# Kernel optimization log

Measured on AMD Instinct MI355X. Metric: run time of the kernel, lower is better.

## Reference

```python
import jax, jax.numpy as jnp
import numpy as np

B, C4, N, L4 = 8, 64, 512, 12
CQ = C4 // 4  # conv output channels


def setup_inputs() -> dict:
    key = jax.random.key(0)
    k_x, k_wc, k_bc, k_wg, k_bg = jax.random.split(key, 5)
    x = jax.random.normal(k_x, (B, C4, N, L4), dtype=jnp.float32)
    # Conv2d(in_dim, in_dim//4, kernel_size=(1,1)) -> pointwise: weight (CQ, C4)
    W_conv = jax.random.normal(k_wc, (CQ, C4), dtype=jnp.float32) / np.sqrt(C4)
    b_conv = jax.random.normal(k_bc, (CQ,), dtype=jnp.float32) * 0.01
    # Linear(in_dim, in_dim)
    W_gcn = jax.random.normal(k_wg, (C4, C4), dtype=jnp.float32) / np.sqrt(C4)
    b_gcn = jax.random.normal(k_bg, (C4,), dtype=jnp.float32) * 0.01
    return {"x": x, "W_conv": W_conv, "b_conv": b_conv, "W_gcn": W_gcn, "b_gcn": b_gcn}


def reference(x, W_conv, b_conv, W_gcn, b_gcn):
    # --- SpatioTemporalCorrelationComputation ---
    # 1x1 conv over channels: (b,c4,n,l) -> (b,cq,n,l)
    Fc = jnp.einsum('oc,bcnl->bonl', W_conv, x) + b_conv[None, :, None, None]
    Fl = Fc[:, :, :, -1]                                   # b,cq,n (last time step)
    xy = jnp.einsum('bcn,bcmt->bnmt', Fl, Fc)              # b,n,n,l4
    xx = jnp.sqrt(jnp.einsum('bcn,bcn->bc', Fl, Fl))       # b,cq
    yy = jnp.sqrt(jnp.einsum('bcnt,bcnt->bc', Fc, Fc))     # b,cq
    l2 = jnp.einsum('bc,bc->b', xx, yy)[:, None, None, None]
    S = xy / l2                                            # b,n,n,l4

    # --- RelationalFeatureExtraction ---
    # Loop-based R[:, :, :, k] = sum_j S[:,k,None,:,j] * F4[:,:,:,j]
    # is exactly this single contraction (Se expansion never materialized):
    R = jnp.einsum('bknj,bcnj->bcnk', S, x)                # b,c4,n,n

    # --- GraphOperation ---
    A = jax.nn.relu(jnp.tanh(jnp.max(R, axis=1)))          # b,n,n
    xg = jnp.einsum('bcnk,bkn->bck', R, A)                 # b,c4,n
    # Linear over channel dim: Fg[b,o,k] = sum_c xg[b,c,k] W[o,c] + bias[o]
    Fg = jnp.einsum('bck,oc->bok', xg, W_gcn) + b_gcn[None, :, None]
    return Fg[..., None]                                   # b,c4,n,1
```

## Files before the change

### kernel.cpp

```cpp
#include <hip/hip_runtime.h>
#include <hip/hip_bf16.h>
#include <math.h>

#define B    8
#define C4   64
#define CQ   16
#define NN   512
#define L4   12
#define XSP  100

#define O_TH   0
#define O_TL   (O_TH + (size_t)B*1024*NN/2)
#define O_FL   (O_TL + (size_t)B*1024*NN/2)
#define O_XX   (O_FL + (size_t)B*CQ*NN)
#define O_YY   (O_XX + B*CQ)
#define O_AH   (O_YY + B*CQ)
#define O_AL   (O_AH + (size_t)B*NN*NN/2)
#define O_FCG  (O_AL + (size_t)B*NN*NN/2)

typedef __attribute__((ext_vector_type(8))) short short8;
typedef __attribute__((ext_vector_type(4))) float floatx4;
typedef __attribute__((ext_vector_type(16))) float floatx16;

__device__ inline void split2(float x0, float x1, uint& hw, uint& lw) {
  uint u0 = __float_as_uint(x0), u1 = __float_as_uint(x1);
  uint h0 = u0 >> 16, h1 = u1 >> 16;
  float r0 = x0 - __uint_as_float(h0 << 16);
  float r1 = x1 - __uint_as_float(h1 << 16);
  hw = h0 | (h1 << 16);
  lw = (__float_as_uint(r0) >> 16) | ((__float_as_uint(r1) >> 16) << 16);
}

__global__ __launch_bounds__(256) void k1a_fc(const float* __restrict__ x,
                                              const float* __restrict__ Wc,
                                              const float* __restrict__ bc,
                                              float* __restrict__ ws) {
  int id = blockIdx.x;
  int b = id & 7;
  int nch = id >> 3;
  int n0 = nch * 8;
  int t = threadIdx.x;
  __shared__ __align__(16) float xs[C4*XSP];
  __shared__ float wcs[CQ*65];
  __shared__ float bcs[CQ];
  __shared__ __align__(16) float fcs[8*CQ*L4];

  for (int e = t; e < CQ*C4; e += 256) {
    int q = e >> 6, c = e & 63;
    wcs[q*65 + c] = Wc[e];
  }
  if (t < CQ) bcs[t] = bc[t];
  const float* xb = x + (size_t)b*C4*NN*L4 + (size_t)n0*L4;
  for (int f = t; f < C4*24; f += 256) {
    int c = f / 24, r = f - c*24;
    float4 v = *(const float4*)(xb + (size_t)c*NN*L4 + r*4);
    *(float4*)(xs + c*XSP + r*4) = v;
  }
  __syncthreads();
  {
    int q = t & 15, slot = t >> 4;
    float accv[6];
    #pragma unroll
    for (int i = 0; i < 6; ++i) accv[i] = bcs[q];
    for (int c = 0; c < C4; ++c) {
      float wv = wcs[q*65 + c];
      const float* xc = xs + c*XSP;
      #pragma unroll
      for (int i = 0; i < 6; ++i) accv[i] += wv * xc[slot + 16*i];
    }
    #pragma unroll
    for (int i = 0; i < 6; ++i) {
      int nj = slot + 16*i;
      int nl = nj / L4, j = nj - nl*L4;
      fcs[nl*(CQ*L4) + q*L4 + j] = accv[i];
      if (j == L4-1) ws[O_FL + ((size_t)b*CQ + q)*NN + n0 + nl] = accv[i];
    }
  }
  __syncthreads();
  if (t < CQ) {
    float yy = 0.f, xx = 0.f;
    for (int nl = 0; nl < 8; ++nl) {
      #pragma unroll
      for (int j = 0; j < L4; ++j) { float v = fcs[nl*(CQ*L4) + t*L4 + j]; yy += v*v; }
      float w = fcs[nl*(CQ*L4) + t*L4 + (L4-1)];
      xx += w*w;
    }
    atomicAdd(ws + O_YY + b*CQ + t, yy);
    atomicAdd(ws + O_XX + b*CQ + t, xx);
  }
  float* fcg = ws + O_FCG + (size_t)(b*64 + nch)*1536;
  for (int f = t; f < 384; f += 256)
    *(float4*)(fcg + f*4) = *(const float4*)(fcs + f*4);
}

__global__ __launch_bounds__(256, 2) void k12_TS(const float* __restrict__ x,
                                                 float* __restrict__ ws) {
  int id = blockIdx.x;
  int b = id & 7;
  int nch = id >> 3;
  int n0 = nch * 8;
  int t = threadIdx.x;
  __shared__ __align__(16) float xs[C4*XSP];
  __shared__ __align__(16) float fcs[8*CQ*L4];
  __shared__ __align__(16) ushort t2h[8*1024];
  __shared__ __align__(16) ushort t2l[8*1024];
  __shared__ float l2tmp[CQ];

  const float* xb = x + (size_t)b*C4*NN*L4 + (size_t)n0*L4;
  for (int f = t; f < C4*24; f += 256) {
    int c = f / 24, r = f - c*24;
    float4 v = *(const float4*)(xb + (size_t)c*NN*L4 + r*4);
    *(float4*)(xs + c*XSP + r*4) = v;
  }
  {
    const float* fcg = ws + O_FCG + (size_t)(b*64 + nch)*1536;
    for (int f = t; f < 384; f += 256)
      *(float4*)(fcs + f*4) = *(const float4*)(fcg + f*4);
  }
  if (t < CQ) l2tmp[t] = sqrtf(ws[O_XX + b*CQ + t]) * sqrtf(ws[O_YY + b*CQ + t]);
  __syncthreads();

  int c = t >> 2, q0 = (t & 3) * 4;
  float vals[4][8];
  for (int nl = 0; nl < 8; ++nl) {
    float xr[L4];
    *(float4*)&xr[0] = *(const float4*)(xs + c*XSP + nl*L4);
    *(float4*)&xr[4] = *(const float4*)(xs + c*XSP + nl*L4 + 4);
    *(float4*)&xr[8] = *(const float4*)(xs + c*XSP + nl*L4 + 8);
    float tvp[4];
    #pragma unroll
    for (int i = 0; i < 4; ++i) {
      const float* fq = fcs + nl*(CQ*L4) + (q0+i)*L4;
      float a = 0.f;
      #pragma unroll
      for (int j = 0; j < L4; ++j) a += fq[j] * xr[j];
      tvp[i] = a;
      vals[i][nl] = a;
    }
    uint hw0, lw0, hw1, lw1;
    split2(tvp[0], tvp[1], hw0, lw0);
    split2(tvp[2], tvp[3], hw1, lw1);
    *(uint2*)(t2h + nl*1024 + t*4) = make_uint2(hw0, hw1);
    *(uint2*)(t2l + nl*1024 + t*4) = make_uint2(lw0, lw1);
  }
  ushort* TH = (ushort*)(ws + O_TH);
  ushort* TL = (ushort*)(ws + O_TL);
  #pragma unroll
  for (int i = 0; i < 4; ++i) {
    int m = c*16 + q0 + i;
    uint hw[4], lw[4];
    #pragma unroll
    for (int jj = 0; jj < 4; ++jj)
      split2(vals[i][2*jj], vals[i][2*jj+1], hw[jj], lw[jj]);
    size_t off = ((size_t)b*1024 + m)*NN + n0;
    *(uint4*)(TH + off) = make_uint4(hw[0], hw[1], hw[2], hw[3]);
    *(uint4*)(TL + off) = make_uint4(lw[0], lw[1], lw[2], lw[3]);
  }
  __syncthreads();

  float l2sum = 0.f;
  #pragma unroll
  for (int q = 0; q < CQ; ++q) l2sum += l2tmp[q];
  float l2inv = 1.0f / l2sum;

  int w = t >> 6, lane = t & 63;
  int col = lane & 31, half = lane >> 5;
  const float* flb = ws + O_FL + (size_t)b*CQ*NN;
  short8 bhf[4], blf[4];
  int kcol[4];
  #pragma unroll
  for (int kt = 0; kt < 4; ++kt) {
    kcol[kt] = w*128 + kt*32 + col;
    float f[8];
    #pragma unroll
    for (int e = 0; e < 8; ++e) f[e] = flb[(size_t)(half*8 + e)*NN + kcol[kt]];
    #pragma unroll
    for (int p = 0; p < 4; ++p) {
      uint hw, lw;
      split2(f[2*p], f[2*p+1], hw, lw);
      ((uint*)&bhf[kt])[p] = hw;
      ((uint*)&blf[kt])[p] = lw;
    }
  }
  ushort* AH = (ushort*)(ws + O_AH) + ((size_t)b*NN + n0)*NN;
  ushort* AL = (ushort*)(ws + O_AL) + ((size_t)b*NN + n0)*NN;

  for (int i = 0; i < 8; ++i) {
    short8 ah[2], al[2];
    #pragma unroll
    for (int ct = 0; ct < 2; ++ct) {
      int off = i*1024 + (ct*32 + col)*16 + half*8;
      ah[ct] = *(const short8*)(t2h + off);
      al[ct] = *(const short8*)(t2l + off);
    }
    #pragma unroll
    for (int kt = 0; kt < 4; ++kt) {
      floatx16 acc[2];
      #pragma unroll
      for (int ct = 0; ct < 2; ++ct) {
        floatx16 a = {0.f,0.f,0.f,0.f,0.f,0.f,0.f,0.f,
                      0.f,0.f,0.f,0.f,0.f,0.f,0.f,0.f};
        a = __builtin_amdgcn_mfma_f32_32x32x16_bf16(ah[ct], bhf[kt], a, 0, 0, 0);
        a = __builtin_amdgcn_mfma_f32_32x32x16_bf16(ah[ct], blf[kt], a, 0, 0, 0);
        a = __builtin_amdgcn_mfma_f32_32x32x16_bf16(al[ct], bhf[kt], a, 0, 0, 0);
        acc[ct] = a;
      }
      float m = acc[0][0];
      #pragma unroll
      for (int ct = 0; ct < 2; ++ct)
        #pragma unroll
        for (int rg = 0; rg < 16; ++rg)
          if (ct + rg) m = fmaxf(m, acc[ct][rg]);
      m = fmaxf(m, __shfl_xor(m, 32));
      float xp = fmaxf(m * l2inv, 0.f);
      float av = 1.f - __fdividef(2.f, __expf(2.f * xp) + 1.f);
      uint u = __float_as_uint(av);
      uint hh = u >> 16;
      float r = av - __uint_as_float(hh << 16);
      ushort lv = (ushort)(__float_as_uint(r) >> 16);
      if (half == 0) {
        AH[(size_t)i*NN + kcol[kt]] = (ushort)hh;
        AL[(size_t)i*NN + kcol[kt]] = lv;
      }
    }
  }
}

__global__ __launch_bounds__(256, 2) void k3_mfma(const float* __restrict__ Wg,
                                                  const float* __restrict__ bg,
                                                  float* __restrict__ ws,
                                                  float* __restrict__ out) {
  int id = blockIdx.x;
  int b = id & 7;
  int rest = id >> 3;
  int kb = rest & 7;
  int mbb = rest >> 3;
  int t = threadIdx.x;
  int lane = t & 63;
  int w = t >> 6;
  int mw = w >> 1, kw = w & 1;
  int row = lane & 15, quad = lane >> 4;

  __shared__ __align__(16) ushort Ah[128*32];
  __shared__ __align__(16) ushort Al[128*32];
  __shared__ __align__(16) ushort Bh[64*32];
  __shared__ __align__(16) ushort Bl[64*32];
  __shared__ float l2tmp[CQ];
  __shared__ float wgs[C4*8];
  __shared__ float xg_s[8][64];

  if (t < CQ) l2tmp[t] = sqrtf(ws[O_XX + b*CQ + t]) * sqrtf(ws[O_YY + b*CQ + t]);
  for (int e = t; e < C4*8; e += 256) {
    int o = e >> 3, cl = e & 7;
    wgs[e] = Wg[o*C4 + mbb*8 + cl];
  }

  const ushort* TH = (const ushort*)(ws + O_TH) + ((size_t)b*1024 + mbb*128)*NN;
  const ushort* TL = (const ushort*)(ws + O_TL) + ((size_t)b*1024 + mbb*128)*NN;
  const ushort* AHp = (const ushort*)(ws + O_AH) + ((size_t)b*NN + kb*64)*NN;
  const ushort* ALp = (const ushort*)(ws + O_AL) + ((size_t)b*NN + kb*64)*NN;

  floatx4 acc[4][2];
  #pragma unroll
  for (int i = 0; i < 4; ++i)
    #pragma unroll
    for (int j = 0; j < 2; ++j) acc[i][j] = (floatx4){0.f, 0.f, 0.f, 0.f};

  for (int ksx = 0; ksx < 16; ++ksx) {
    int p0 = ksx*32;
    __syncthreads();
    #pragma unroll
    for (int i = 0; i < 2; ++i) {
      int f = t + 256*i;
      int m = f >> 2, seg = (f & 3) * 8;
      *(uint4*)(Ah + m*32 + seg) = *(const uint4*)(TH + (size_t)m*NN + p0 + seg);
      *(uint4*)(Al + m*32 + seg) = *(const uint4*)(TL + (size_t)m*NN + p0 + seg);
    }
    {
      int j = t >> 2, seg = (t & 3) * 8;
      *(uint4*)(Bh + j*32 + seg) = *(const uint4*)(AHp + (size_t)j*NN + p0 + seg);
      *(uint4*)(Bl + j*32 + seg) = *(const uint4*)(ALp + (size_t)j*NN + p0 + seg);
    }
    __syncthreads();
    short8 bh[2], bl[2];
    #pragma unroll
    for (int kt = 0; kt < 2; ++kt) {
      int jrow = kw*32 + kt*16 + row;
      bh[kt] = *(const short8*)(Bh + jrow*32 + quad*8);
      bl[kt] = *(const short8*)(Bl + jrow*32 + quad*8);
    }
    #pragma unroll
    for (int mt = 0; mt < 4; ++mt) {
      int mrow = mw*64 + mt*16 + row;
      short8 ah = *(const short8*)(Ah + mrow*32 + quad*8);
      short8 al = *(const short8*)(Al + mrow*32 + quad*8);
      #pragma unroll
      for (int kt = 0; kt < 2; ++kt) {
        acc[mt][kt] = __builtin_amdgcn_mfma_f32_16x16x32_bf16(ah, bh[kt], acc[mt][kt], 0, 0, 0);
        acc[mt][kt] = __builtin_amdgcn_mfma_f32_16x16x32_bf16(ah, bl[kt], acc[mt][kt], 0, 0, 0);
        acc[mt][kt] = __builtin_amdgcn_mfma_f32_16x16x32_bf16(al, bh[kt], acc[mt][kt], 0, 0, 0);
      }
    }
  }
  float l2sum = 0.f;
  #pragma unroll
  for (int q = 0; q < CQ; ++q) l2sum += l2tmp[q];
  float l2inv = 1.0f / l2sum;

  const float* flb = ws + O_FL + (size_t)b*CQ*NN;
  float fl[2][4];
  #pragma unroll
  for (int kt = 0; kt < 2; ++kt) {
    int kcol = kb*64 + kw*32 + kt*16 + row;
    #pragma unroll
    for (int rg = 0; rg < 4; ++rg)
      fl[kt][rg] = flb[(size_t)(quad*4 + rg)*NN + kcol];
  }
  #pragma unroll
  for (int mt = 0; mt < 4; ++mt) {
    #pragma unroll
    for (int kt = 0; kt < 2; ++kt) {
      float s = fl[kt][0]*acc[mt][kt][0] + fl[kt][1]*acc[mt][kt][1]
              + fl[kt][2]*acc[mt][kt][2] + fl[kt][3]*acc[mt][kt][3];
      s += __shfl_xor(s, 32);
      s += __shfl_xor(s, 16);
      if (quad == 0)
        xg_s[mw*4 + mt][kw*32 + kt*16 + row] = s * l2inv;
    }
  }
  __syncthreads();
  int kl = t & 63, og = t >> 6;
  #pragma unroll
  for (int oi = 0; oi < 16; ++oi) {
    int o = og*16 + oi;
    float a = 0.f;
    #pragma unroll
    for (int cl = 0; cl < 8; ++cl) a += wgs[o*8 + cl] * xg_s[cl][kl];
    if (mbb == 0) a += bg[o];
    atomicAdd(out + ((size_t)(b*C4 + o))*NN + kb*64 + kl, a);
  }
}

extern "C" void kernel_launch(void* const* d_in, const int* in_sizes, int n_in,
                              void* d_out, int out_size, void* d_ws, size_t ws_size,
                              hipStream_t stream) {
  const float* x  = (const float*)d_in[0];
  const float* Wc = (const float*)d_in[1];
  const float* bc = (const float*)d_in[2];
  const float* Wg = (const float*)d_in[3];
  const float* bg = (const float*)d_in[4];
  float* ws  = (float*)d_ws;
  float* out = (float*)d_out;

  hipMemsetAsync(ws + O_XX, 0, 2*B*CQ*sizeof(float), stream);
  hipMemsetAsync(out, 0, (size_t)out_size, stream);

  k1a_fc <<<B*64,  256, 0, stream>>>(x, Wc, bc, ws);
  k12_TS <<<B*64,  256, 0, stream>>>(x, ws);
  k3_mfma<<<B*64,  256, 0, stream>>>(Wg, bg, ws, out);
}
```

Measured before the change: 140.6 us.

## Halve per-block work and double grid size across all three kernels

```diff
diff --git a/kernel.cpp b/kernel.cpp
--- a/kernel.cpp
+++ b/kernel.cpp
@@ -7,7 +7,7 @@
 #define CQ   16
 #define NN   512
 #define L4   12
-#define XSP  100
+#define XS4  52
 
 #define O_TH   0
 #define O_TL   (O_TH + (size_t)B*1024*NN/2)
@@ -31,19 +31,19 @@
   lw = (__float_as_uint(r0) >> 16) | ((__float_as_uint(r1) >> 16) << 16);
 }
 
-__global__ __launch_bounds__(256) void k1a_fc(const float* __restrict__ x,
-                                              const float* __restrict__ Wc,
-                                              const float* __restrict__ bc,
-                                              float* __restrict__ ws) {
+__global__ __launch_bounds__(256, 4) void k1a_fc(const float* __restrict__ x,
+                                                 const float* __restrict__ Wc,
+                                                 const float* __restrict__ bc,
+                                                 float* __restrict__ ws) {
   int id = blockIdx.x;
   int b = id & 7;
   int nch = id >> 3;
-  int n0 = nch * 8;
+  int n0 = nch * 4;
   int t = threadIdx.x;
-  __shared__ __align__(16) float xs[C4*XSP];
+  __shared__ __align__(16) float xs[C4*XS4];
   __shared__ float wcs[CQ*65];
   __shared__ float bcs[CQ];
-  __shared__ __align__(16) float fcs[8*CQ*L4];
+  __shared__ __align__(16) float fcs[4*CQ*L4];
 
   for (int e = t; e < CQ*C4; e += 256) {
     int q = e >> 6, c = e & 63;
@@ -51,25 +51,25 @@
   }
   if (t < CQ) bcs[t] = bc[t];
   const float* xb = x + (size_t)b*C4*NN*L4 + (size_t)n0*L4;
-  for (int f = t; f < C4*24; f += 256) {
-    int c = f / 24, r = f - c*24;
+  for (int f = t; f < C4*12; f += 256) {
+    int c = f / 12, r = f - c*12;
     float4 v = *(const float4*)(xb + (size_t)c*NN*L4 + r*4);
-    *(float4*)(xs + c*XSP + r*4) = v;
+    *(float4*)(xs + c*XS4 + r*4) = v;
   }
   __syncthreads();
   {
     int q = t & 15, slot = t >> 4;
-    float accv[6];
-    #pragma unroll
-    for (int i = 0; i < 6; ++i) accv[i] = bcs[q];
+    float accv[3];
+    #pragma unroll
+    for (int i = 0; i < 3; ++i) accv[i] = bcs[q];
     for (int c = 0; c < C4; ++c) {
       float wv = wcs[q*65 + c];
-      const float* xc = xs + c*XSP;
-      #pragma unroll
-      for (int i = 0; i < 6; ++i) accv[i] += wv * xc[slot + 16*i];
-    }
-    #pragma unroll
-    for (int i = 0; i < 6; ++i) {
+      const float* xc = xs + c*XS4;
+      #pragma unroll
+      for (int i = 0; i < 3; ++i) accv[i] += wv * xc[slot + 16*i];
+    }
+    #pragma unroll
+    for (int i = 0; i < 3; ++i) {
       int nj = slot + 16*i;
       int nl = nj / L4, j = nj - nl*L4;
       fcs[nl*(CQ*L4) + q*L4 + j] = accv[i];
@@ -79,7 +79,7 @@
   __syncthreads();
   if (t < CQ) {
     float yy = 0.f, xx = 0.f;
-    for (int nl = 0; nl < 8; ++nl) {
+    for (int nl = 0; nl < 4; ++nl) {
       #pragma unroll
       for (int j = 0; j < L4; ++j) { float v = fcs[nl*(CQ*L4) + t*L4 + j]; yy += v*v; }
       float w = fcs[nl*(CQ*L4) + t*L4 + (L4-1)];
@@ -88,45 +88,45 @@
     atomicAdd(ws + O_YY + b*CQ + t, yy);
     atomicAdd(ws + O_XX + b*CQ + t, xx);
   }
-  float* fcg = ws + O_FCG + (size_t)(b*64 + nch)*1536;
-  for (int f = t; f < 384; f += 256)
-    *(float4*)(fcg + f*4) = *(const float4*)(fcs + f*4);
-}
-
-__global__ __launch_bounds__(256, 2) void k12_TS(const float* __restrict__ x,
+  float* fcg = ws + O_FCG + (size_t)(b*128 + nch)*768;
+  if (t < 192)
+    *(float4*)(fcg + t*4) = *(const float4*)(fcs + t*4);
+}
+
+__global__ __launch_bounds__(256, 4) void k12_TS(const float* __restrict__ x,
                                                  float* __restrict__ ws) {
   int id = blockIdx.x;
   int b = id & 7;
   int nch = id >> 3;
-  int n0 = nch * 8;
+  int n0 = nch * 4;
   int t = threadIdx.x;
-  __shared__ __align__(16) float xs[C4*XSP];
-  __shared__ __align__(16) float fcs[8*CQ*L4];
-  __shared__ __align__(16) ushort t2h[8*1024];
-  __shared__ __align__(16) ushort t2l[8*1024];
+  __shared__ __align__(16) float xs[C4*XS4];
+  __shared__ __align__(16) float fcs[4*CQ*L4];
+  __shared__ __align__(16) ushort t2h[4*1024];
+  __shared__ __align__(16) ushort t2l[4*1024];
   __shared__ float l2tmp[CQ];
 
   const float* xb = x + (size_t)b*C4*NN*L4 + (size_t)n0*L4;
-  for (int f = t; f < C4*24; f += 256) {
-    int c = f / 24, r = f - c*24;
+  for (int f = t; f < C4*12; f += 256) {
+    int c = f / 12, r = f - c*12;
     float4 v = *(const float4*)(xb + (size_t)c*NN*L4 + r*4);
-    *(float4*)(xs + c*XSP + r*4) = v;
+    *(float4*)(xs + c*XS4 + r*4) = v;
   }
   {
-    const float* fcg = ws + O_FCG + (size_t)(b*64 + nch)*1536;
-    for (int f = t; f < 384; f += 256)
-      *(float4*)(fcs + f*4) = *(const float4*)(fcg + f*4);
+    const float* fcg = ws + O_FCG + (size_t)(b*128 + nch)*768;
+    if (t < 192)
+      *(float4*)(fcs + t*4) = *(const float4*)(fcg + t*4);
   }
   if (t < CQ) l2tmp[t] = sqrtf(ws[O_XX + b*CQ + t]) * sqrtf(ws[O_YY + b*CQ + t]);
   __syncthreads();
 
   int c = t >> 2, q0 = (t & 3) * 4;
-  float vals[4][8];
-  for (int nl = 0; nl < 8; ++nl) {
+  float vals[4][4];
+  for (int nl = 0; nl < 4; ++nl) {
     float xr[L4];
-    *(float4*)&xr[0] = *(const float4*)(xs + c*XSP + nl*L4);
-    *(float4*)&xr[4] = *(const float4*)(xs + c*XSP + nl*L4 + 4);
-    *(float4*)&xr[8] = *(const float4*)(xs + c*XSP + nl*L4 + 8);
+    *(float4*)&xr[0] = *(const float4*)(xs + c*XS4 + nl*L4);
+    *(float4*)&xr[4] = *(const float4*)(xs + c*XS4 + nl*L4 + 4);
+    *(float4*)&xr[8] = *(const float4*)(xs + c*XS4 + nl*L4 + 8);
     float tvp[4];
     #pragma unroll
     for (int i = 0; i < 4; ++i) {
@@ -148,13 +148,12 @@
   #pragma unroll
   for (int i = 0; i < 4; ++i) {
     int m = c*16 + q0 + i;
-    uint hw[4], lw[4];
-    #pragma unroll
-    for (int jj = 0; jj < 4; ++jj)
-      split2(vals[i][2*jj], vals[i][2*jj+1], hw[jj], lw[jj]);
+    uint hw0, lw0, hw1, lw1;
+    split2(vals[i][0], vals[i][1], hw0, lw0);
+    split2(vals[i][2], vals[i][3], hw1, lw1);
     size_t off = ((size_t)b*1024 + m)*NN + n0;
-    *(uint4*)(TH + off) = make_uint4(hw[0], hw[1], hw[2], hw[3]);
-    *(uint4*)(TL + off) = make_uint4(lw[0], lw[1], lw[2], lw[3]);
+    *(uint2*)(TH + off) = make_uint2(hw0, hw1);
+    *(uint2*)(TL + off) = make_uint2(lw0, lw1);
   }
   __syncthreads();
 
@@ -185,7 +184,7 @@
   ushort* AH = (ushort*)(ws + O_AH) + ((size_t)b*NN + n0)*NN;
   ushort* AL = (ushort*)(ws + O_AL) + ((size_t)b*NN + n0)*NN;
 
-  for (int i = 0; i < 8; ++i) {
+  for (int i = 0; i < 4; ++i) {
     short8 ah[2], al[2];
     #pragma unroll
     for (int ct = 0; ct < 2; ++ct) {
@@ -226,15 +225,17 @@
   }
 }
 
-__global__ __launch_bounds__(256, 2) void k3_mfma(const float* __restrict__ Wg,
+__global__ __launch_bounds__(256, 4) void k3_mfma(const float* __restrict__ Wg,
                                                   const float* __restrict__ bg,
                                                   float* __restrict__ ws,
                                                   float* __restrict__ out) {
   int id = blockIdx.x;
   int b = id & 7;
   int rest = id >> 3;
-  int kb = rest & 7;
-  int mbb = rest >> 3;
+  int nh = rest & 1;
+  int rest2 = rest >> 1;
+  int kb = rest2 & 7;
+  int mbb = rest2 >> 3;
   int t = threadIdx.x;
   int lane = t & 63;
   int w = t >> 6;
@@ -266,7 +267,7 @@
     #pragma unroll
     for (int j = 0; j < 2; ++j) acc[i][j] = (floatx4){0.f, 0.f, 0.f, 0.f};
 
-  for (int ksx = 0; ksx < 16; ++ksx) {
+  for (int ksx = nh*8; ksx < nh*8 + 8; ++ksx) {
     int p0 = ksx*32;
     __syncthreads();
     #pragma unroll
@@ -336,7 +337,7 @@
     float a = 0.f;
     #pragma unroll
     for (int cl = 0; cl < 8; ++cl) a += wgs[o*8 + cl] * xg_s[cl][kl];
-    if (mbb == 0) a += bg[o];
+    if (mbb == 0 && nh == 0) a += bg[o];
     atomicAdd(out + ((size_t)(b*C4 + o))*NN + kb*64 + kl, a);
   }
 }
@@ -355,7 +356,7 @@
   hipMemsetAsync(ws + O_XX, 0, 2*B*CQ*sizeof(float), stream);
   hipMemsetAsync(out, 0, (size_t)out_size, stream);
 
-  k1a_fc <<<B*64,  256, 0, stream>>>(x, Wc, bc, ws);
-  k12_TS <<<B*64,  256, 0, stream>>>(x, ws);
-  k3_mfma<<<B*64,  256, 0, stream>>>(Wg, bg, ws, out);
-}
+  k1a_fc <<<B*128, 256, 0, stream>>>(x, Wc, bc, ws);
+  k12_TS <<<B*128, 256, 0, stream>>>(x, ws);
+  k3_mfma<<<B*128, 256, 0, stream>>>(Wg, bg, ws, out);
+}
```

New measurement: 181.7 us. 1.29x slower.
